# Performance work log

Hardware: AMD Instinct MI355X
Metric: run time of the kernel (lower is better)

Reference implementation:

```python
import jax, jax.numpy as jnp
import numpy as np

H = 2048            # hidden_size
INTER = 8192        # intermediate_size
E = 16              # num_experts
V = 32000           # vocab_size
I = INTER // E      # per-expert intermediate (tp_size=1) = 512
N = 4096            # num_tokens
BASE_ROUTING_SCALE = 10.0


def setup_inputs() -> dict:
    key = jax.random.key(0)
    ks = jax.random.split(key, 6)
    x = jax.random.normal(ks[0], (N, H), dtype=jnp.float32)
    token_ids = jax.random.randint(ks[1], (N,), 0, V)
    mu = jax.random.normal(ks[2], (N, H), dtype=jnp.float32)
    # kaiming-uniform-ish scaled params
    gate_up_proj = jax.random.normal(ks[3], (E, H, 2 * I), dtype=jnp.float32) * (1.0 / np.sqrt(H))
    down_proj = jax.random.normal(ks[4], (E, I, H), dtype=jnp.float32) * (1.0 / np.sqrt(I))
    # mu_router initialized to zeros in the module; use small random so routing is actually mu-biased
    mu_router_w = jax.random.normal(ks[5], (E, H), dtype=jnp.float32) * 0.02
    return {"x": x, "token_ids": token_ids, "mu": mu,
            "gate_up_proj": gate_up_proj, "down_proj": down_proj,
            "mu_router_w": mu_router_w}


def reference(x, token_ids, mu, gate_up_proj, down_proj, mu_router_w):
    # --- routing: expert = token_id % E, biased by mu logits ---
    base = jnp.clip(token_ids, 0, V - 1) % E              # [N]
    logits = (jax.nn.one_hot(base, E, dtype=jnp.float32) * BASE_ROUTING_SCALE
              + mu @ mu_router_w.T)                       # [N, E]
    expert_ids = jnp.argmax(logits, axis=-1)              # [N]

    Iloc = gate_up_proj.shape[-1] // 2

    # --- grouped expert SwiGLU MLP: scan over experts, mask-combine outputs ---
    def step(acc, inp):
        wg, wd, e = inp
        gu = x @ wg                                       # [N, 2I]
        h = jax.nn.silu(gu[:, :Iloc]) * gu[:, Iloc:]      # [N, I]
        o = h @ wd                                        # [N, H]
        acc = acc + jnp.where((expert_ids == e)[:, None], o, 0.0)
        return acc, None

    out0 = jnp.zeros_like(x)
    out, _ = jax.lax.scan(step, out0, (gate_up_proj, down_proj, jnp.arange(E)))
    return out
```

## Files before the change

### kernel.cpp

```cpp
#include <hip/hip_runtime.h>
#include <hip/hip_bf16.h>

#define NT 4096
#define HD 2048
#define NE 16
#define ID 512
#define TWO_I 1024
#define PITCH 72
#define MAXITEMS 47

typedef __attribute__((ext_vector_type(8))) short bf16x8_t;
typedef __attribute__((ext_vector_type(4))) float f32x4_t;

__device__ __forceinline__ unsigned short f2bf(float f) {
  union { float f; unsigned int u; } v; v.f = f;
  unsigned int r = v.u + 0x7fffu + ((v.u >> 16) & 1u);
  return (unsigned short)(r >> 16);
}
__device__ __forceinline__ unsigned pk2(unsigned short a, unsigned short b) {
  return (unsigned)a | ((unsigned)b << 16);
}
__device__ __forceinline__ void gl_lds16(const void* g, void* l) {
  __builtin_amdgcn_global_load_lds(
      (const __attribute__((address_space(1))) unsigned int*)g,
      (__attribute__((address_space(3))) unsigned int*)l, 16, 0, 0);
}

__global__ void k_cast_x(const float* __restrict__ x, unsigned short* __restrict__ xb) {
  size_t i = ((size_t)blockIdx.x * 256 + threadIdx.x) * 8;
  float4 a = *(const float4*)(x + i);
  float4 b = *(const float4*)(x + i + 4);
  uint4 pk;
  pk.x = pk2(f2bf(a.x), f2bf(a.y)); pk.y = pk2(f2bf(a.z), f2bf(a.w));
  pk.z = pk2(f2bf(b.x), f2bf(b.y)); pk.w = pk2(f2bf(b.z), f2bf(b.w));
  *(uint4*)(xb + i) = pk;
}

__global__ void k_route(const float* __restrict__ mu, const int* __restrict__ tok,
                        const float* __restrict__ wr, int* __restrict__ eid) {
  int t = blockIdx.x;
  int tid = threadIdx.x;
  float p[NE];
#pragma unroll
  for (int e = 0; e < NE; ++e) p[e] = 0.f;
  const float* m = mu + (size_t)t * HD;
  for (int h = tid; h < HD; h += 256) {
    float mv = m[h];
#pragma unroll
    for (int e = 0; e < NE; ++e) p[e] += mv * wr[e * HD + h];
  }
#pragma unroll
  for (int e = 0; e < NE; ++e) {
    float v = p[e];
#pragma unroll
    for (int s = 32; s; s >>= 1) v += __shfl_xor(v, s, 64);
    p[e] = v;
  }
  __shared__ float red[4][NE];
  int lane = tid & 63, wv = tid >> 6;
  if (lane == 0) {
#pragma unroll
    for (int e = 0; e < NE; ++e) red[wv][e] = p[e];
  }
  __syncthreads();
  if (tid == 0) {
    int tk = tok[t];
    if (tk < 0) tk = 0;
    if (tk > 31999) tk = 31999;
    int base = tk & 15;
    float best = -3.0e38f; int bi = 0;
    for (int e = 0; e < NE; ++e) {
      float v = red[0][e] + red[1][e] + red[2][e] + red[3][e];
      if (e == base) v += 10.0f;
      if (v > best) { best = v; bi = e; }
    }
    eid[t] = bi;
  }
}

__global__ void k_init(int* counts, int* cursors) {
  int i = threadIdx.x;
  if (i < NE) { counts[i] = 0; cursors[i] = 0; }
}
__global__ void k_hist(const int* __restrict__ eid, int* __restrict__ counts) {
  int t = blockIdx.x * 256 + threadIdx.x;
  if (t < NT) atomicAdd(&counts[eid[t]], 1);
}
__global__ void k_scan(const int* __restrict__ counts, int* __restrict__ offsets,
                       int* __restrict__ cursors, int* __restrict__ wk) {
  if (threadIdx.x == 0) {
    int s = 0;
    for (int e = 0; e < NE; ++e) { offsets[e] = s; cursors[e] = s; s += counts[e]; }
    offsets[NE] = s;
    int n = 0;
    for (int e = 0; e < NE; ++e) {
      int tiles = (counts[e] + 127) >> 7;
      for (int m = 0; m < tiles; ++m) { wk[n++] = e | (m << 8); }
    }
    wk[MAXITEMS] = n;
  }
}
__global__ void k_scatter(const int* __restrict__ eid, int* __restrict__ cursors,
                          int* __restrict__ tlist) {
  int t = blockIdx.x * 256 + threadIdx.x;
  if (t < NT) {
    int e = eid[t];
    int pos = atomicAdd(&cursors[e], 1);
    tlist[pos] = t;
  }
}

__global__ __launch_bounds__(256, 3) void k_gemm1(
    const unsigned short* __restrict__ xb, const float* __restrict__ gup,
    const int* __restrict__ offsets, const int* __restrict__ tlist,
    const int* __restrict__ wk, unsigned short* __restrict__ hbuf) {
  int item = blockIdx.y;
  if (item >= wk[MAXITEMS]) return;
  int w = wk[item];
  int e = w & 255, tb = (w >> 8) * 128;
  int off = offsets[e], cnt = offsets[e + 1] - off;
  int c0 = blockIdx.x * 32;

  __shared__ float Bbuf[2][64 * 64];
  __shared__ unsigned short Pbuf[64 * PITCH];
  __shared__ int ltok[128];

  int tid = threadIdx.x, lane = tid & 63, wv = tid >> 6;
  if (tid < 128) { int r = tb + tid; if (r > cnt - 1) r = cnt - 1; ltok[tid] = tlist[off + r]; }
  __syncthreads();

  int lr = lane & 15, hi = lane >> 4, mb = wv * 32;
  const unsigned short* aRow0 = xb + (size_t)ltok[mb + lr] * HD + hi * 8;
  const unsigned short* aRow1 = xb + (size_t)ltok[mb + 16 + lr] * HD + hi * 8;

  const float* bSrc[4];
  int bDst[4];
  {
    int cc = lane & 15;
    int gcol = (cc < 8) ? (c0 + cc * 4) : (ID + c0 + (cc - 8) * 4);
    const float* Wg = gup + (size_t)e * HD * TWO_I;
#pragma unroll
    for (int i = 0; i < 4; ++i) {
      int kr = wv * 16 + i * 4 + (lane >> 4);
      bSrc[i] = Wg + (size_t)kr * TWO_I + gcol;
      bDst[i] = (wv * 16 + i * 4) * 64;
    }
  }
  auto stageB = [&](int buf) {
#pragma unroll
    for (int i = 0; i < 4; ++i) { gl_lds16(bSrc[i], &Bbuf[buf][bDst[i]]); bSrc[i] += (size_t)64 * TWO_I; }
  };

  stageB(0);

  f32x4_t zero = {0.f, 0.f, 0.f, 0.f};
  f32x4_t accg[2][2], accu[2][2];
#pragma unroll
  for (int m = 0; m < 2; ++m)
#pragma unroll
    for (int n = 0; n < 2; ++n) { accg[m][n] = zero; accu[m][n] = zero; }

  for (int kt = 0; kt < 32; ++kt) {
    int cur = kt & 1;
    __builtin_amdgcn_s_barrier();
    bf16x8_t a00, a01, a10, a11;
    a00 = *(const bf16x8_t*)(aRow0 + kt * 64);
    a01 = *(const bf16x8_t*)(aRow0 + kt * 64 + 32);
    a10 = *(const bf16x8_t*)(aRow1 + kt * 64);
    a11 = *(const bf16x8_t*)(aRow1 + kt * 64 + 32);
    __builtin_amdgcn_sched_barrier(0);
    if (kt < 31) stageB(cur ^ 1);
    __builtin_amdgcn_sched_barrier(0);
    if (kt < 31) asm volatile("s_waitcnt vmcnt(4)" ::: "memory");
    else         asm volatile("s_waitcnt vmcnt(0)" ::: "memory");
    __builtin_amdgcn_sched_barrier(0);
    __builtin_amdgcn_s_barrier();

    {
      int c = lane, ks = wv;
      unsigned short tmp[16];
#pragma unroll
      for (int j = 0; j < 16; ++j) tmp[j] = f2bf(Bbuf[cur][(ks * 16 + j) * 64 + c]);
      uint4 p0, p1;
      p0.x = pk2(tmp[0], tmp[1]);   p0.y = pk2(tmp[2], tmp[3]);
      p0.z = pk2(tmp[4], tmp[5]);   p0.w = pk2(tmp[6], tmp[7]);
      p1.x = pk2(tmp[8], tmp[9]);   p1.y = pk2(tmp[10], tmp[11]);
      p1.z = pk2(tmp[12], tmp[13]); p1.w = pk2(tmp[14], tmp[15]);
      *(uint4*)&Pbuf[c * PITCH + ks * 16] = p0;
      *(uint4*)&Pbuf[c * PITCH + ks * 16 + 8] = p1;
    }
    asm volatile("s_waitcnt lgkmcnt(0)" ::: "memory");
    __builtin_amdgcn_sched_barrier(0);
    __builtin_amdgcn_s_barrier();

    __builtin_amdgcn_s_setprio(1);
#pragma unroll
    for (int kk = 0; kk < 2; ++kk) {
      int klo = kk * 32 + hi * 8;
      bf16x8_t bg[2], bu[2];
#pragma unroll
      for (int n = 0; n < 2; ++n) {
        bg[n] = *(bf16x8_t*)&Pbuf[(n * 16 + lr) * PITCH + klo];
        bu[n] = *(bf16x8_t*)&Pbuf[(32 + n * 16 + lr) * PITCH + klo];
      }
      bf16x8_t a0 = kk ? a01 : a00;
      bf16x8_t a1 = kk ? a11 : a10;
#pragma unroll
      for (int n = 0; n < 2; ++n) {
        accg[0][n] = __builtin_amdgcn_mfma_f32_16x16x32_bf16(a0, bg[n], accg[0][n], 0, 0, 0);
        accu[0][n] = __builtin_amdgcn_mfma_f32_16x16x32_bf16(a0, bu[n], accu[0][n], 0, 0, 0);
        accg[1][n] = __builtin_amdgcn_mfma_f32_16x16x32_bf16(a1, bg[n], accg[1][n], 0, 0, 0);
        accu[1][n] = __builtin_amdgcn_mfma_f32_16x16x32_bf16(a1, bu[n], accu[1][n], 0, 0, 0);
      }
    }
    __builtin_amdgcn_s_setprio(0);
  }

  int rq = hi * 4;
#pragma unroll
  for (int m = 0; m < 2; ++m)
#pragma unroll
    for (int n = 0; n < 2; ++n)
#pragma unroll
      for (int j = 0; j < 4; ++j) {
        int r = tb + mb + m * 16 + rq + j;
        if (r < cnt) {
          float g = accg[m][n][j], u = accu[m][n][j];
          float hv = (g / (1.f + __expf(-g))) * u;
          hbuf[(size_t)(off + r) * ID + c0 + n * 16 + lr] = f2bf(hv);
        }
      }
}

__global__ __launch_bounds__(256, 3) void k_gemm2(
    const unsigned short* __restrict__ hbuf, const float* __restrict__ dwn,
    const int* __restrict__ offsets, const int* __restrict__ tlist,
    const int* __restrict__ wk, float* __restrict__ out) {
  int item = blockIdx.y;
  if (item >= wk[MAXITEMS]) return;
  int w = wk[item];
  int e = w & 255, tb = (w >> 8) * 128;
  int off = offsets[e], cnt = offsets[e + 1] - off;
  int c0 = blockIdx.x * 64;

  __shared__ float Bbuf[2][64 * 64];
  __shared__ unsigned short Pbuf[64 * PITCH];

  int tid = threadIdx.x, lane = tid & 63, wv = tid >> 6;
  int lr = lane & 15, hi = lane >> 4, mb = wv * 32;

  int r0 = tb + mb + lr;      if (r0 > cnt - 1) r0 = cnt - 1;
  int r1 = tb + mb + 16 + lr; if (r1 > cnt - 1) r1 = cnt - 1;
  const unsigned short* aRow0 = hbuf + (size_t)(off + r0) * ID + hi * 8;
  const unsigned short* aRow1 = hbuf + (size_t)(off + r1) * ID + hi * 8;

  const float* bSrc[4];
  int bDst[4];
  {
    int cc = lane & 15;
    const float* Wd = dwn + (size_t)e * ID * HD;
#pragma unroll
    for (int i = 0; i < 4; ++i) {
      int kr = wv * 16 + i * 4 + (lane >> 4);
      bSrc[i] = Wd + (size_t)kr * HD + c0 + cc * 4;
      bDst[i] = (wv * 16 + i * 4) * 64;
    }
  }
  auto stageB = [&](int buf) {
#pragma unroll
    for (int i = 0; i < 4; ++i) { gl_lds16(bSrc[i], &Bbuf[buf][bDst[i]]); bSrc[i] += (size_t)64 * HD; }
  };

  stageB(0);

  f32x4_t zero = {0.f, 0.f, 0.f, 0.f};
  f32x4_t acc[2][4];
#pragma unroll
  for (int m = 0; m < 2; ++m)
#pragma unroll
    for (int n = 0; n < 4; ++n) acc[m][n] = zero;

  for (int kt = 0; kt < 8; ++kt) {
    int cur = kt & 1;
    __builtin_amdgcn_s_barrier();
    bf16x8_t a00, a01, a10, a11;
    a00 = *(const bf16x8_t*)(aRow0 + kt * 64);
    a01 = *(const bf16x8_t*)(aRow0 + kt * 64 + 32);
    a10 = *(const bf16x8_t*)(aRow1 + kt * 64);
    a11 = *(const bf16x8_t*)(aRow1 + kt * 64 + 32);
    __builtin_amdgcn_sched_barrier(0);
    if (kt < 7) stageB(cur ^ 1);
    __builtin_amdgcn_sched_barrier(0);
    if (kt < 7) asm volatile("s_waitcnt vmcnt(4)" ::: "memory");
    else        asm volatile("s_waitcnt vmcnt(0)" ::: "memory");
    __builtin_amdgcn_sched_barrier(0);
    __builtin_amdgcn_s_barrier();

    {
      int c = lane, ks = wv;
      unsigned short tmp[16];
#pragma unroll
      for (int j = 0; j < 16; ++j) tmp[j] = f2bf(Bbuf[cur][(ks * 16 + j) * 64 + c]);
      uint4 p0, p1;
      p0.x = pk2(tmp[0], tmp[1]);   p0.y = pk2(tmp[2], tmp[3]);
      p0.z = pk2(tmp[4], tmp[5]);   p0.w = pk2(tmp[6], tmp[7]);
      p1.x = pk2(tmp[8], tmp[9]);   p1.y = pk2(tmp[10], tmp[11]);
      p1.z = pk2(tmp[12], tmp[13]); p1.w = pk2(tmp[14], tmp[15]);
      *(uint4*)&Pbuf[c * PITCH + ks * 16] = p0;
      *(uint4*)&Pbuf[c * PITCH + ks * 16 + 8] = p1;
    }
    asm volatile("s_waitcnt lgkmcnt(0)" ::: "memory");
    __builtin_amdgcn_sched_barrier(0);
    __builtin_amdgcn_s_barrier();

    __builtin_amdgcn_s_setprio(1);
#pragma unroll
    for (int kk = 0; kk < 2; ++kk) {
      int klo = kk * 32 + hi * 8;
      bf16x8_t b[4];
#pragma unroll
      for (int n = 0; n < 4; ++n) b[n] = *(bf16x8_t*)&Pbuf[(n * 16 + lr) * PITCH + klo];
      bf16x8_t a0 = kk ? a01 : a00;
      bf16x8_t a1 = kk ? a11 : a10;
#pragma unroll
      for (int n = 0; n < 4; ++n) {
        acc[0][n] = __builtin_amdgcn_mfma_f32_16x16x32_bf16(a0, b[n], acc[0][n], 0, 0, 0);
        acc[1][n] = __builtin_amdgcn_mfma_f32_16x16x32_bf16(a1, b[n], acc[1][n], 0, 0, 0);
      }
    }
    __builtin_amdgcn_s_setprio(0);
  }

  int rq = hi * 4;
#pragma unroll
  for (int m = 0; m < 2; ++m)
#pragma unroll
    for (int n = 0; n < 4; ++n)
#pragma unroll
      for (int j = 0; j < 4; ++j) {
        int r = tb + mb + m * 16 + rq + j;
        if (r < cnt) {
          out[(size_t)tlist[off + r] * HD + c0 + n * 16 + lr] = acc[m][n][j];
        }
      }
}

extern "C" void kernel_launch(void* const* d_in, const int* in_sizes, int n_in,
                              void* d_out, int out_size, void* d_ws, size_t ws_size,
                              hipStream_t stream) {
  (void)in_sizes; (void)n_in; (void)out_size; (void)ws_size;
  const float* x   = (const float*)d_in[0];
  const int*   tok = (const int*)d_in[1];
  const float* mu  = (const float*)d_in[2];
  const float* gup = (const float*)d_in[3];
  const float* dwn = (const float*)d_in[4];
  const float* wr  = (const float*)d_in[5];
  float* out = (float*)d_out;

  char* ws = (char*)d_ws;
  int* eid     = (int*)ws;
  int* tlist   = (int*)(ws + 16384);
  int* counts  = (int*)(ws + 32768);
  int* offsets = (int*)(ws + 32896);
  int* cursors = (int*)(ws + 33024);
  int* wk      = (int*)(ws + 33152);
  unsigned short* xb   = (unsigned short*)(ws + 65536);
  unsigned short* hbuf = (unsigned short*)(ws + 65536 + (size_t)NT * HD * 2);

  k_cast_x <<<4096, 256, 0, stream>>>(x, xb);
  k_route  <<<NT, 256, 0, stream>>>(mu, tok, wr, eid);
  k_init   <<<1, 64, 0, stream>>>(counts, cursors);
  k_hist   <<<16, 256, 0, stream>>>(eid, counts);
  k_scan   <<<1, 64, 0, stream>>>(counts, offsets, cursors, wk);
  k_scatter<<<16, 256, 0, stream>>>(eid, cursors, tlist);
  k_gemm1  <<<dim3(16, MAXITEMS), 256, 0, stream>>>(xb, gup, offsets, tlist, wk, hbuf);
  k_gemm2  <<<dim3(32, MAXITEMS), 256, 0, stream>>>(hbuf, dwn, offsets, tlist, wk, out);
}
```

Baseline: 202.8 us.

## Deepen GEMM pipelines with double-buffered Pbuf and two-stage A/B prefetch

Both expert GEMM kernels now double-buffer the transposed bf16 B tile (Pbuf) and keep two register sets of A fragments. Global loads for step k+2 are issued right after step k's MFMAs, instead of one step ahead. The per-step synchronisation drops from three barriers to one, and vmcnt waits let one full stage of loads stay in flight. This is meant to hide global-load latency and barrier stalls, at the cost of more LDS, more registers and a longer unrolled prologue and steady-state.

New measurement: 201.3 us. Within noise of the previous version (-0.8%).

```diff
diff --git a/kernel.cpp b/kernel.cpp
--- a/kernel.cpp
+++ b/kernel.cpp
@@ -122,7 +122,7 @@
   int c0 = blockIdx.x * 32;
 
   __shared__ float Bbuf[2][64 * 64];
-  __shared__ unsigned short Pbuf[64 * PITCH];
+  __shared__ unsigned short Pbuf[2][64 * PITCH];
   __shared__ int ltok[128];
 
   int tid = threadIdx.x, lane = tid & 63, wv = tid >> 6;
@@ -146,12 +146,32 @@
       bDst[i] = (wv * 16 + i * 4) * 64;
     }
   }
-  auto stageB = [&](int buf) {
-#pragma unroll
-    for (int i = 0; i < 4; ++i) { gl_lds16(bSrc[i], &Bbuf[buf][bDst[i]]); bSrc[i] += (size_t)64 * TWO_I; }
-  };
-
-  stageB(0);
+
+#define STAGEB(BUF) do { \
+  _Pragma("unroll") for (int i = 0; i < 4; ++i) { \
+    gl_lds16(bSrc[i], &Bbuf[BUF][bDst[i]]); bSrc[i] += (size_t)64 * TWO_I; } \
+} while (0)
+
+  bf16x8_t A0[4], A1[4];
+#define LOADA(SET, KT) do { \
+  SET[0] = *(const bf16x8_t*)(aRow0 + (KT) * 64); \
+  SET[1] = *(const bf16x8_t*)(aRow0 + (KT) * 64 + 32); \
+  SET[2] = *(const bf16x8_t*)(aRow1 + (KT) * 64); \
+  SET[3] = *(const bf16x8_t*)(aRow1 + (KT) * 64 + 32); \
+} while (0)
+
+#define TRANSP(BUF) do { \
+  const float* s_ = &Bbuf[BUF][(wv * 16) * 64 + lane]; \
+  unsigned short t_[16]; \
+  _Pragma("unroll") for (int j = 0; j < 16; ++j) t_[j] = f2bf(s_[j * 64]); \
+  uint4 q0_, q1_; \
+  q0_.x = pk2(t_[0], t_[1]);   q0_.y = pk2(t_[2], t_[3]); \
+  q0_.z = pk2(t_[4], t_[5]);   q0_.w = pk2(t_[6], t_[7]); \
+  q1_.x = pk2(t_[8], t_[9]);   q1_.y = pk2(t_[10], t_[11]); \
+  q1_.z = pk2(t_[12], t_[13]); q1_.w = pk2(t_[14], t_[15]); \
+  *(uint4*)&Pbuf[BUF][lane * PITCH + wv * 16] = q0_; \
+  *(uint4*)&Pbuf[BUF][lane * PITCH + wv * 16 + 8] = q1_; \
+} while (0)
 
   f32x4_t zero = {0.f, 0.f, 0.f, 0.f};
   f32x4_t accg[2][2], accu[2][2];
@@ -160,61 +180,53 @@
 #pragma unroll
     for (int n = 0; n < 2; ++n) { accg[m][n] = zero; accu[m][n] = zero; }
 
-  for (int kt = 0; kt < 32; ++kt) {
-    int cur = kt & 1;
-    __builtin_amdgcn_s_barrier();
-    bf16x8_t a00, a01, a10, a11;
-    a00 = *(const bf16x8_t*)(aRow0 + kt * 64);
-    a01 = *(const bf16x8_t*)(aRow0 + kt * 64 + 32);
-    a10 = *(const bf16x8_t*)(aRow1 + kt * 64);
-    a11 = *(const bf16x8_t*)(aRow1 + kt * 64 + 32);
-    __builtin_amdgcn_sched_barrier(0);
-    if (kt < 31) stageB(cur ^ 1);
-    __builtin_amdgcn_sched_barrier(0);
-    if (kt < 31) asm volatile("s_waitcnt vmcnt(4)" ::: "memory");
-    else         asm volatile("s_waitcnt vmcnt(0)" ::: "memory");
-    __builtin_amdgcn_sched_barrier(0);
-    __builtin_amdgcn_s_barrier();
-
-    {
-      int c = lane, ks = wv;
-      unsigned short tmp[16];
-#pragma unroll
-      for (int j = 0; j < 16; ++j) tmp[j] = f2bf(Bbuf[cur][(ks * 16 + j) * 64 + c]);
-      uint4 p0, p1;
-      p0.x = pk2(tmp[0], tmp[1]);   p0.y = pk2(tmp[2], tmp[3]);
-      p0.z = pk2(tmp[4], tmp[5]);   p0.w = pk2(tmp[6], tmp[7]);
-      p1.x = pk2(tmp[8], tmp[9]);   p1.y = pk2(tmp[10], tmp[11]);
-      p1.z = pk2(tmp[12], tmp[13]); p1.w = pk2(tmp[14], tmp[15]);
-      *(uint4*)&Pbuf[c * PITCH + ks * 16] = p0;
-      *(uint4*)&Pbuf[c * PITCH + ks * 16 + 8] = p1;
-    }
-    asm volatile("s_waitcnt lgkmcnt(0)" ::: "memory");
-    __builtin_amdgcn_sched_barrier(0);
-    __builtin_amdgcn_s_barrier();
-
-    __builtin_amdgcn_s_setprio(1);
-#pragma unroll
-    for (int kk = 0; kk < 2; ++kk) {
-      int klo = kk * 32 + hi * 8;
-      bf16x8_t bg[2], bu[2];
-#pragma unroll
-      for (int n = 0; n < 2; ++n) {
-        bg[n] = *(bf16x8_t*)&Pbuf[(n * 16 + lr) * PITCH + klo];
-        bu[n] = *(bf16x8_t*)&Pbuf[(32 + n * 16 + lr) * PITCH + klo];
-      }
-      bf16x8_t a0 = kk ? a01 : a00;
-      bf16x8_t a1 = kk ? a11 : a10;
-#pragma unroll
-      for (int n = 0; n < 2; ++n) {
-        accg[0][n] = __builtin_amdgcn_mfma_f32_16x16x32_bf16(a0, bg[n], accg[0][n], 0, 0, 0);
-        accu[0][n] = __builtin_amdgcn_mfma_f32_16x16x32_bf16(a0, bu[n], accu[0][n], 0, 0, 0);
-        accg[1][n] = __builtin_amdgcn_mfma_f32_16x16x32_bf16(a1, bg[n], accg[1][n], 0, 0, 0);
-        accu[1][n] = __builtin_amdgcn_mfma_f32_16x16x32_bf16(a1, bu[n], accu[1][n], 0, 0, 0);
-      }
-    }
-    __builtin_amdgcn_s_setprio(0);
-  }
+#define MFMA_PH(BUF, SET) do { \
+  __builtin_amdgcn_s_setprio(1); \
+  _Pragma("unroll") for (int kk = 0; kk < 2; ++kk) { \
+    int klo = kk * 32 + hi * 8; \
+    bf16x8_t bg0 = *(bf16x8_t*)&Pbuf[BUF][(lr) * PITCH + klo]; \
+    bf16x8_t bg1 = *(bf16x8_t*)&Pbuf[BUF][(16 + lr) * PITCH + klo]; \
+    bf16x8_t bu0 = *(bf16x8_t*)&Pbuf[BUF][(32 + lr) * PITCH + klo]; \
+    bf16x8_t bu1 = *(bf16x8_t*)&Pbuf[BUF][(48 + lr) * PITCH + klo]; \
+    bf16x8_t a0 = SET[kk], a1 = SET[2 + kk]; \
+    accg[0][0] = __builtin_amdgcn_mfma_f32_16x16x32_bf16(a0, bg0, accg[0][0], 0, 0, 0); \
+    accg[0][1] = __builtin_amdgcn_mfma_f32_16x16x32_bf16(a0, bg1, accg[0][1], 0, 0, 0); \
+    accu[0][0] = __builtin_amdgcn_mfma_f32_16x16x32_bf16(a0, bu0, accu[0][0], 0, 0, 0); \
+    accu[0][1] = __builtin_amdgcn_mfma_f32_16x16x32_bf16(a0, bu1, accu[0][1], 0, 0, 0); \
+    accg[1][0] = __builtin_amdgcn_mfma_f32_16x16x32_bf16(a1, bg0, accg[1][0], 0, 0, 0); \
+    accg[1][1] = __builtin_amdgcn_mfma_f32_16x16x32_bf16(a1, bg1, accg[1][1], 0, 0, 0); \
+    accu[1][0] = __builtin_amdgcn_mfma_f32_16x16x32_bf16(a1, bu0, accu[1][0], 0, 0, 0); \
+    accu[1][1] = __builtin_amdgcn_mfma_f32_16x16x32_bf16(a1, bu1, accu[1][1], 0, 0, 0); \
+  } \
+  __builtin_amdgcn_s_setprio(0); \
+} while (0)
+
+#define SUBSTEP(KT, BUF, SET, VMC) do { \
+  asm volatile("s_waitcnt vmcnt(" #VMC ")" ::: "memory"); \
+  __builtin_amdgcn_sched_barrier(0); \
+  TRANSP(BUF); \
+  asm volatile("s_waitcnt lgkmcnt(0)" ::: "memory"); \
+  __builtin_amdgcn_sched_barrier(0); \
+  __builtin_amdgcn_s_barrier(); \
+  MFMA_PH(BUF, SET); \
+  if ((KT) + 2 < 32) { LOADA(SET, (KT) + 2); STAGEB(BUF); } \
+} while (0)
+
+  LOADA(A0, 0); STAGEB(0);
+  LOADA(A1, 1); STAGEB(1);
+
+  for (int kt2 = 0; kt2 < 15; ++kt2) {
+    SUBSTEP(2 * kt2, 0, A0, 8);
+    SUBSTEP(2 * kt2 + 1, 1, A1, 8);
+  }
+  SUBSTEP(30, 0, A0, 8);
+  SUBSTEP(31, 1, A1, 0);
+
+#undef SUBSTEP
+#undef MFMA_PH
+#undef TRANSP
+#undef LOADA
+#undef STAGEB
 
   int rq = hi * 4;
 #pragma unroll
@@ -244,7 +256,7 @@
   int c0 = blockIdx.x * 64;
 
   __shared__ float Bbuf[2][64 * 64];
-  __shared__ unsigned short Pbuf[64 * PITCH];
+  __shared__ unsigned short Pbuf[2][64 * PITCH];
 
   int tid = threadIdx.x, lane = tid & 63, wv = tid >> 6;
   int lr = lane & 15, hi = lane >> 4, mb = wv * 32;
@@ -266,12 +278,32 @@
       bDst[i] = (wv * 16 + i * 4) * 64;
     }
   }
-  auto stageB = [&](int buf) {
-#pragma unroll
-    for (int i = 0; i < 4; ++i) { gl_lds16(bSrc[i], &Bbuf[buf][bDst[i]]); bSrc[i] += (size_t)64 * HD; }
-  };
-
-  stageB(0);
+
+#define STAGEB(BUF) do { \
+  _Pragma("unroll") for (int i = 0; i < 4; ++i) { \
+    gl_lds16(bSrc[i], &Bbuf[BUF][bDst[i]]); bSrc[i] += (size_t)64 * HD; } \
+} while (0)
+
+  bf16x8_t A0[4], A1[4];
+#define LOADA(SET, KT) do { \
+  SET[0] = *(const bf16x8_t*)(aRow0 + (KT) * 64); \
+  SET[1] = *(const bf16x8_t*)(aRow0 + (KT) * 64 + 32); \
+  SET[2] = *(const bf16x8_t*)(aRow1 + (KT) * 64); \
+  SET[3] = *(const bf16x8_t*)(aRow1 + (KT) * 64 + 32); \
+} while (0)
+
+#define TRANSP(BUF) do { \
+  const float* s_ = &Bbuf[BUF][(wv * 16) * 64 + lane]; \
+  unsigned short t_[16]; \
+  _Pragma("unroll") for (int j = 0; j < 16; ++j) t_[j] = f2bf(s_[j * 64]); \
+  uint4 q0_, q1_; \
+  q0_.x = pk2(t_[0], t_[1]);   q0_.y = pk2(t_[2], t_[3]); \
+  q0_.z = pk2(t_[4], t_[5]);   q0_.w = pk2(t_[6], t_[7]); \
+  q1_.x = pk2(t_[8], t_[9]);   q1_.y = pk2(t_[10], t_[11]); \
+  q1_.z = pk2(t_[12], t_[13]); q1_.w = pk2(t_[14], t_[15]); \
+  *(uint4*)&Pbuf[BUF][lane * PITCH + wv * 16] = q0_; \
+  *(uint4*)&Pbuf[BUF][lane * PITCH + wv * 16 + 8] = q1_; \
+} while (0)
 
   f32x4_t zero = {0.f, 0.f, 0.f, 0.f};
   f32x4_t acc[2][4];
@@ -280,56 +312,55 @@
 #pragma unroll
     for (int n = 0; n < 4; ++n) acc[m][n] = zero;
 
-  for (int kt = 0; kt < 8; ++kt) {
-    int cur = kt & 1;
-    __builtin_amdgcn_s_barrier();
-    bf16x8_t a00, a01, a10, a11;
-    a00 = *(const bf16x8_t*)(aRow0 + kt * 64);
-    a01 = *(const bf16x8_t*)(aRow0 + kt * 64 + 32);
-    a10 = *(const bf16x8_t*)(aRow1 + kt * 64);
-    a11 = *(const bf16x8_t*)(aRow1 + kt * 64 + 32);
-    __builtin_amdgcn_sched_barrier(0);
-    if (kt < 7) stageB(cur ^ 1);
-    __builtin_amdgcn_sched_barrier(0);
-    if (kt < 7) asm volatile("s_waitcnt vmcnt(4)" ::: "memory");
-    else        asm volatile("s_waitcnt vmcnt(0)" ::: "memory");
-    __builtin_amdgcn_sched_barrier(0);
-    __builtin_amdgcn_s_barrier();
-
-    {
-      int c = lane, ks = wv;
-      unsigned short tmp[16];
-#pragma unroll
-      for (int j = 0; j < 16; ++j) tmp[j] = f2bf(Bbuf[cur][(ks * 16 + j) * 64 + c]);
-      uint4 p0, p1;
-      p0.x = pk2(tmp[0], tmp[1]);   p0.y = pk2(tmp[2], tmp[3]);
-      p0.z = pk2(tmp[4], tmp[5]);   p0.w = pk2(tmp[6], tmp[7]);
-      p1.x = pk2(tmp[8], tmp[9]);   p1.y = pk2(tmp[10], tmp[11]);
-      p1.z = pk2(tmp[12], tmp[13]); p1.w = pk2(tmp[14], tmp[15]);
-      *(uint4*)&Pbuf[c * PITCH + ks * 16] = p0;
-      *(uint4*)&Pbuf[c * PITCH + ks * 16 + 8] = p1;
-    }
-    asm volatile("s_waitcnt lgkmcnt(0)" ::: "memory");
-    __builtin_amdgcn_sched_barrier(0);
-    __builtin_amdgcn_s_barrier();
-
-    __builtin_amdgcn_s_setprio(1);
-#pragma unroll
-    for (int kk = 0; kk < 2; ++kk) {
-      int klo = kk * 32 + hi * 8;
-      bf16x8_t b[4];
-#pragma unroll
-      for (int n = 0; n < 4; ++n) b[n] = *(bf16x8_t*)&Pbuf[(n * 16 + lr) * PITCH + klo];
-      bf16x8_t a0 = kk ? a01 : a00;
-      bf16x8_t a1 = kk ? a11 : a10;
-#pragma unroll
-      for (int n = 0; n < 4; ++n) {
-        acc[0][n] = __builtin_amdgcn_mfma_f32_16x16x32_bf16(a0, b[n], acc[0][n], 0, 0, 0);
-        acc[1][n] = __builtin_amdgcn_mfma_f32_16x16x32_bf16(a1, b[n], acc[1][n], 0, 0, 0);
-      }
-    }
-    __builtin_amdgcn_s_setprio(0);
-  }
+#define MFMA_PH(BUF, SET) do { \
+  __builtin_amdgcn_s_setprio(1); \
+  _Pragma("unroll") for (int kk = 0; kk < 2; ++kk) { \
+    int klo = kk * 32 + hi * 8; \
+    bf16x8_t b0 = *(bf16x8_t*)&Pbuf[BUF][(lr) * PITCH + klo]; \
+    bf16x8_t b1 = *(bf16x8_t*)&Pbuf[BUF][(16 + lr) * PITCH + klo]; \
+    bf16x8_t b2 = *(bf16x8_t*)&Pbuf[BUF][(32 + lr) * PITCH + klo]; \
+    bf16x8_t b3 = *(bf16x8_t*)&Pbuf[BUF][(48 + lr) * PITCH + klo]; \
+    bf16x8_t a0 = SET[kk], a1 = SET[2 + kk]; \
+    acc[0][0] = __builtin_amdgcn_mfma_f32_16x16x32_bf16(a0, b0, acc[0][0], 0, 0, 0); \
+    acc[0][1] = __builtin_amdgcn_mfma_f32_16x16x32_bf16(a0, b1, acc[0][1], 0, 0, 0); \
+    acc[0][2] = __builtin_amdgcn_mfma_f32_16x16x32_bf16(a0, b2, acc[0][2], 0, 0, 0); \
+    acc[0][3] = __builtin_amdgcn_mfma_f32_16x16x32_bf16(a0, b3, acc[0][3], 0, 0, 0); \
+    acc[1][0] = __builtin_amdgcn_mfma_f32_16x16x32_bf16(a1, b0, acc[1][0], 0, 0, 0); \
+    acc[1][1] = __builtin_amdgcn_mfma_f32_16x16x32_bf16(a1, b1, acc[1][1], 0, 0, 0); \
+    acc[1][2] = __builtin_amdgcn_mfma_f32_16x16x32_bf16(a1, b2, acc[1][2], 0, 0, 0); \
+    acc[1][3] = __builtin_amdgcn_mfma_f32_16x16x32_bf16(a1, b3, acc[1][3], 0, 0, 0); \
+  } \
+  __builtin_amdgcn_s_setprio(0); \
+} while (0)
+
+#define SUBSTEP(KT, BUF, SET, VMC) do { \
+  asm volatile("s_waitcnt vmcnt(" #VMC ")" ::: "memory"); \
+  __builtin_amdgcn_sched_barrier(0); \
+  TRANSP(BUF); \
+  asm volatile("s_waitcnt lgkmcnt(0)" ::: "memory"); \
+  __builtin_amdgcn_sched_barrier(0); \
+  __builtin_amdgcn_s_barrier(); \
+  MFMA_PH(BUF, SET); \
+  if ((KT) + 2 < 8) { LOADA(SET, (KT) + 2); STAGEB(BUF); } \
+} while (0)
+
+  LOADA(A0, 0); STAGEB(0);
+  LOADA(A1, 1); STAGEB(1);
+
+  SUBSTEP(0, 0, A0, 8);
+  SUBSTEP(1, 1, A1, 8);
+  SUBSTEP(2, 0, A0, 8);
+  SUBSTEP(3, 1, A1, 8);
+  SUBSTEP(4, 0, A0, 8);
+  SUBSTEP(5, 1, A1, 8);
+  SUBSTEP(6, 0, A0, 8);
+  SUBSTEP(7, 1, A1, 0);
+
+#undef SUBSTEP
+#undef MFMA_PH
+#undef TRANSP
+#undef LOADA
+#undef STAGEB
 
   int rq = hi * 4;
 #pragma unroll
```
